# Optimization experiments

Hardware: AMD Instinct MI355X
Metric: run time of the kernel (lower is better)

The kernel has to match this reference:

```python
import jax, jax.numpy as jnp
import numpy as np

B, H, S, D = 4, 16, 4096, 64

def _phi(x):
    # feature map for linear attention: elu(x) + 1 (positive features)
    return jax.nn.elu(x) + 1.0

def setup_inputs() -> dict:
    key = jax.random.key(0)
    kq, kk, kv = jax.random.split(key, 3)
    return {
        "query": jax.random.normal(kq, (B, H, S, D), dtype=jnp.float32),
        "key": jax.random.normal(kk, (B, H, S, D), dtype=jnp.float32),
        "value": jax.random.normal(kv, (B, H, S, D), dtype=jnp.float32),
        "attention_mask": jnp.ones((B, S), dtype=jnp.float32),
    }

def reference(query, key, value, attention_mask):
    head_dim = query.shape[-1]
    scale = 1.0 / jnp.sqrt(jnp.sqrt(jnp.float32(head_dim)))
    q = query * scale
    k = key * scale
    phi_q = _phi(q)
    phi_k = _phi(k)
    m = attention_mask[:, None, :, None]  # [B,1,S,1]
    phi_q = phi_q * m
    phi_k = phi_k * m
    # kv_term: [B,H,D,Dv]
    kv_term = jnp.einsum("bhsd,bhse->bhde", phi_k, value)
    out = jnp.einsum("bhsd,bhde->bhse", phi_q, kv_term)
    # normalizer: phi_q @ sum_s phi_k -> [B,H,S,1]
    k_one = jnp.sum(phi_k, axis=-2)  # [B,H,D]
    normalizer = jnp.einsum("bhsd,bhd->bhs", phi_q, k_one)[..., None]
    return out / (normalizer + 1e-8)
```

## Files before the change

kernel.cpp:

```cpp
#include <hip/hip_runtime.h>

#define BDIM 4
#define HDIM 16
#define SDIM 4096
#define DDIM 64
#define NBH (BDIM * HDIM)

#define P1_TS 16
#define BH_STRIDE (DDIM * DDIM + DDIM)
#define CHUNK_FLOATS (NBH * BH_STRIDE)
#define P2_MT 128

__device__ __forceinline__ float phi_f(float x) {
    return x > 0.0f ? x + 1.0f : __expf(x);
}

template<bool ATOMIC>
__global__ __launch_bounds__(256) void la_phase1(
    const float* __restrict__ K, const float* __restrict__ V,
    const float* __restrict__ mask, float* __restrict__ outp, int chunk_rows)
{
    __shared__ float kT[2][P1_TS][DDIM];
    __shared__ float vT[2][P1_TS][DDIM];

    const int bh  = blockIdx.y;
    const int b   = bh / HDIM;
    const int t   = threadIdx.x;
    const int row = t >> 4;
    const int c4  = (t & 15) << 2;
    const int d0  = row << 2;
    const int e0  = c4;
    const int s_base = blockIdx.x * chunk_rows;

    const float* Kb = K + (size_t)bh * SDIM * DDIM;
    const float* Vb = V + (size_t)bh * SDIM * DDIM;
    const float* mb = mask + (size_t)b * SDIM;

    const float scale = 0.35355339059327373f;

    float acc[4][4] = {};
    float k1[4] = {0.f, 0.f, 0.f, 0.f};

    int s0 = s_base + row;
    float4 kf = *(const float4*)(Kb + (size_t)s0 * DDIM + c4);
    float4 vf = *(const float4*)(Vb + (size_t)s0 * DDIM + c4);
    float  m  = mb[s0];

    const int ntiles = chunk_rows >> 4;
    int p = 0;
    for (int tt = 0; tt < ntiles; ++tt) {
        const float p0 = phi_f(kf.x * scale) * m;
        const float p1 = phi_f(kf.y * scale) * m;
        const float p2 = phi_f(kf.z * scale) * m;
        const float p3 = phi_f(kf.w * scale) * m;
        kT[p][row][c4 + 0] = p0;
        kT[p][row][c4 + 1] = p1;
        kT[p][row][c4 + 2] = p2;
        kT[p][row][c4 + 3] = p3;
        *(float4*)&vT[p][row][c4] = vf;
        k1[0] += p0; k1[1] += p1; k1[2] += p2; k1[3] += p3;
        __syncthreads();

        if (tt + 1 < ntiles) {
            const int sn = s_base + ((tt + 1) << 4) + row;
            kf = *(const float4*)(Kb + (size_t)sn * DDIM + c4);
            vf = *(const float4*)(Vb + (size_t)sn * DDIM + c4);
            m  = mb[sn];
        }

        #pragma unroll
        for (int ss = 0; ss < P1_TS; ++ss) {
            const float4 a  = *(const float4*)&kT[p][ss][d0];
            const float4 v4 = *(const float4*)&vT[p][ss][e0];
            acc[0][0] += a.x * v4.x; acc[0][1] += a.x * v4.y; acc[0][2] += a.x * v4.z; acc[0][3] += a.x * v4.w;
            acc[1][0] += a.y * v4.x; acc[1][1] += a.y * v4.y; acc[1][2] += a.y * v4.z; acc[1][3] += a.y * v4.w;
            acc[2][0] += a.z * v4.x; acc[2][1] += a.z * v4.y; acc[2][2] += a.z * v4.z; acc[2][3] += a.z * v4.w;
            acc[3][0] += a.w * v4.x; acc[3][1] += a.w * v4.y; acc[3][2] += a.w * v4.z; acc[3][3] += a.w * v4.w;
        }
        p ^= 1;
    }

    float* base = ATOMIC ? (outp + (size_t)bh * BH_STRIDE)
                         : (outp + ((size_t)blockIdx.x * NBH + bh) * BH_STRIDE);
    if (ATOMIC) {
        #pragma unroll
        for (int i = 0; i < 4; ++i)
            #pragma unroll
            for (int j = 0; j < 4; ++j)
                atomicAdd(&base[(d0 + i) * DDIM + e0 + j], acc[i][j]);
    } else {
        #pragma unroll
        for (int i = 0; i < 4; ++i)
            *(float4*)&base[(d0 + i) * DDIM + e0] =
                make_float4(acc[i][0], acc[i][1], acc[i][2], acc[i][3]);
    }

    __syncthreads();
    kT[0][row][c4 + 0] = k1[0];
    kT[0][row][c4 + 1] = k1[1];
    kT[0][row][c4 + 2] = k1[2];
    kT[0][row][c4 + 3] = k1[3];
    __syncthreads();
    if (t < DDIM) {
        float s1 = 0.f;
        #pragma unroll
        for (int r = 0; r < P1_TS; ++r) s1 += kT[0][r][t];
        if (ATOMIC) atomicAdd(&base[DDIM * DDIM + t], s1);
        else        base[DDIM * DDIM + t] = s1;
    }
}

__global__ __launch_bounds__(256) void la_reduce(
    const float* __restrict__ part, float* __restrict__ fin, int nc)
{
    const int g = blockIdx.x * 256 + threadIdx.x;
    const float4* p4 = (const float4*)part;
    float4 s = p4[g];
    for (int c = 1; c < nc; ++c) {
        const float4 v = p4[(size_t)c * (CHUNK_FLOATS / 4) + g];
        s.x += v.x; s.y += v.y; s.z += v.z; s.w += v.w;
    }
    ((float4*)fin)[g] = s;
}

__global__ __launch_bounds__(512) void la_phase2(
    const float* __restrict__ Q, const float* __restrict__ mask,
    const float* __restrict__ fin_all, float* __restrict__ out)
{
    __shared__ float kvL[DDIM][DDIM];
    __shared__ float pqT[DDIM][P2_MT + 4];
    __shared__ float koL[DDIM];

    const int bh = blockIdx.y;
    const int b  = bh / HDIM;
    const int t  = threadIdx.x;
    const int s_base = blockIdx.x * P2_MT;

    const float scale = 0.35355339059327373f;
    const float* fin = fin_all + (size_t)bh * BH_STRIDE;

    {
        const float4* src = (const float4*)fin;
        float4* dst = (float4*)&kvL[0][0];
        dst[t] = src[t];
        dst[t + 512] = src[t + 512];
        if (t < DDIM) koL[t] = fin[DDIM * DDIM + t];
    }
    {
        const float* Qb = Q + (size_t)bh * SDIM * DDIM;
        const float* mb = mask + (size_t)b * SDIM;
        const int lr   = t & 15;
        const int c4   = ((t >> 4) & 15) << 2;
        const int half = t >> 8;
        #pragma unroll
        for (int k = 0; k < 4; ++k) {
            const int r = lr + 16 * (half * 4 + k);
            const int s = s_base + r;
            const float4 qf = *(const float4*)(Qb + (size_t)s * DDIM + c4);
            const float mm = mb[s];
            pqT[c4 + 0][r] = phi_f(qf.x * scale) * mm;
            pqT[c4 + 1][r] = phi_f(qf.y * scale) * mm;
            pqT[c4 + 2][r] = phi_f(qf.z * scale) * mm;
            pqT[c4 + 3][r] = phi_f(qf.w * scale) * mm;
        }
    }
    __syncthreads();

    const int r0 = (t >> 4) << 2;
    const int e0 = (t & 15) << 2;
    float acc[4][4] = {};
    float nrm[4] = {0.f, 0.f, 0.f, 0.f};

    #pragma unroll 16
    for (int d = 0; d < DDIM; ++d) {
        const float4 a  = *(const float4*)&pqT[d][r0];
        const float4 bb = *(const float4*)&kvL[d][e0];
        const float ko = koL[d];
        acc[0][0] += a.x * bb.x; acc[0][1] += a.x * bb.y; acc[0][2] += a.x * bb.z; acc[0][3] += a.x * bb.w;
        acc[1][0] += a.y * bb.x; acc[1][1] += a.y * bb.y; acc[1][2] += a.y * bb.z; acc[1][3] += a.y * bb.w;
        acc[2][0] += a.z * bb.x; acc[2][1] += a.z * bb.y; acc[2][2] += a.z * bb.z; acc[2][3] += a.z * bb.w;
        acc[3][0] += a.w * bb.x; acc[3][1] += a.w * bb.y; acc[3][2] += a.w * bb.z; acc[3][3] += a.w * bb.w;
        nrm[0] += a.x * ko; nrm[1] += a.y * ko; nrm[2] += a.z * ko; nrm[3] += a.w * ko;
    }

    float* ob = out + ((size_t)bh * SDIM + s_base) * DDIM;
    #pragma unroll
    for (int i = 0; i < 4; ++i) {
        const float inv = 1.0f / (nrm[i] + 1e-8f);
        float4 o;
        o.x = acc[i][0] * inv;
        o.y = acc[i][1] * inv;
        o.z = acc[i][2] * inv;
        o.w = acc[i][3] * inv;
        *(float4*)(ob + (size_t)(r0 + i) * DDIM + e0) = o;
    }
}

extern "C" void kernel_launch(void* const* d_in, const int* in_sizes, int n_in,
                              void* d_out, int out_size, void* d_ws, size_t ws_size,
                              hipStream_t stream) {
    const float* Q = (const float*)d_in[0];
    const float* K = (const float*)d_in[1];
    const float* V = (const float*)d_in[2];
    const float* M = (const float*)d_in[3];
    float* out = (float*)d_out;

    const size_t chunk_bytes = (size_t)CHUNK_FLOATS * sizeof(float);

    int nc = 0;
    if      (ws_size >= 33 * chunk_bytes) nc = 32;
    else if (ws_size >= 17 * chunk_bytes) nc = 16;

    if (nc > 0) {
        float* part = (float*)d_ws;
        float* fin  = part + (size_t)nc * CHUNK_FLOATS;
        la_phase1<false><<<dim3(nc, NBH), dim3(256), 0, stream>>>(K, V, M, part, SDIM / nc);
        la_reduce<<<dim3(CHUNK_FLOATS / 4 / 256), dim3(256), 0, stream>>>(part, fin, nc);
        la_phase2<<<dim3(SDIM / P2_MT, NBH), dim3(512), 0, stream>>>(Q, M, fin, out);
    } else {
        float* fin = (float*)d_ws;
        hipMemsetAsync(d_ws, 0, chunk_bytes, stream);
        la_phase1<true><<<dim3(16, NBH), dim3(256), 0, stream>>>(K, V, M, fin, SDIM / 16);
        la_phase2<<<dim3(SDIM / P2_MT, NBH), dim3(512), 0, stream>>>(Q, M, fin, out);
    }
}
```

Before: 248.0 us.

## Use 8x8 register tiles and per-wave independent pipelines in both phases

Phase 1 drops to 128 threads, two waves that each own half the chunk. Each wave has its own padded shared-memory tile, so the per-tile block barrier is gone, and each thread accumulates an 8x8 outer product. The two waves combine their results through shared memory at the end. Phase 2 likewise moves to 128 threads with 8x8 per-thread tiles, raising arithmetic intensity per shared-memory load at the cost of more registers and fewer threads per block, which may hurt latency hiding.

```diff
diff --git a/kernel.cpp b/kernel.cpp
--- a/kernel.cpp
+++ b/kernel.cpp
@@ -6,31 +6,41 @@
 #define DDIM 64
 #define NBH (BDIM * HDIM)
 
-#define P1_TS 16
 #define BH_STRIDE (DDIM * DDIM + DDIM)
 #define CHUNK_FLOATS (NBH * BH_STRIDE)
-#define P2_MT 128
+
+#define P1_STRIDE 66
+#define P1_WSZ (2 * 16 * P1_STRIDE)
 
 __device__ __forceinline__ float phi_f(float x) {
     return x > 0.0f ? x + 1.0f : __expf(x);
 }
 
 template<bool ATOMIC>
-__global__ __launch_bounds__(256) void la_phase1(
+__global__ __launch_bounds__(128) void la_phase1(
     const float* __restrict__ K, const float* __restrict__ V,
     const float* __restrict__ mask, float* __restrict__ outp, int chunk_rows)
 {
-    __shared__ float kT[2][P1_TS][DDIM];
-    __shared__ float vT[2][P1_TS][DDIM];
-
-    const int bh  = blockIdx.y;
-    const int b   = bh / HDIM;
-    const int t   = threadIdx.x;
-    const int row = t >> 4;
-    const int c4  = (t & 15) << 2;
-    const int d0  = row << 2;
-    const int e0  = c4;
-    const int s_base = blockIdx.x * chunk_rows;
+    __shared__ float smem[2 * P1_WSZ + 64];
+
+    const int bh = blockIdx.y;
+    const int b  = bh / HDIM;
+    const int t  = threadIdx.x;
+    const int w  = t >> 6;
+    const int l  = t & 63;
+
+    float* kTw = smem + w * P1_WSZ;
+    float* vTw = kTw + 16 * P1_STRIDE;
+    float* k1w = smem + 2 * P1_WSZ;
+
+    const int lr = l & 15;
+    const int cg = (l >> 4) << 2;
+    const int d0 = (l >> 3) << 3;
+    const int e0 = (l & 7) << 3;
+
+    const int rows_per_wave = chunk_rows >> 1;
+    const int s_wave = blockIdx.x * chunk_rows + w * rows_per_wave;
+    const int ntiles = rows_per_wave >> 4;
 
     const float* Kb = K + (size_t)bh * SDIM * DDIM;
     const float* Vb = V + (size_t)bh * SDIM * DDIM;
@@ -38,75 +48,113 @@
 
     const float scale = 0.35355339059327373f;
 
-    float acc[4][4] = {};
-    float k1[4] = {0.f, 0.f, 0.f, 0.f};
-
-    int s0 = s_base + row;
-    float4 kf = *(const float4*)(Kb + (size_t)s0 * DDIM + c4);
-    float4 vf = *(const float4*)(Vb + (size_t)s0 * DDIM + c4);
-    float  m  = mb[s0];
-
-    const int ntiles = chunk_rows >> 4;
-    int p = 0;
+    float acc[8][8] = {};
+    float k1p[4][4] = {};
+
+    float4 kf[4], vf[4];
+    float m;
+    {
+        const int sr = s_wave + lr;
+        #pragma unroll
+        for (int j = 0; j < 4; ++j) {
+            kf[j] = *(const float4*)(Kb + (size_t)sr * DDIM + cg + 16 * j);
+            vf[j] = *(const float4*)(Vb + (size_t)sr * DDIM + cg + 16 * j);
+        }
+        m = mb[sr];
+    }
+
     for (int tt = 0; tt < ntiles; ++tt) {
-        const float p0 = phi_f(kf.x * scale) * m;
-        const float p1 = phi_f(kf.y * scale) * m;
-        const float p2 = phi_f(kf.z * scale) * m;
-        const float p3 = phi_f(kf.w * scale) * m;
-        kT[p][row][c4 + 0] = p0;
-        kT[p][row][c4 + 1] = p1;
-        kT[p][row][c4 + 2] = p2;
-        kT[p][row][c4 + 3] = p3;
-        *(float4*)&vT[p][row][c4] = vf;
-        k1[0] += p0; k1[1] += p1; k1[2] += p2; k1[3] += p3;
-        __syncthreads();
-
+        float p[4][4];
+        #pragma unroll
+        for (int j = 0; j < 4; ++j) {
+            p[j][0] = phi_f(kf[j].x * scale) * m;
+            p[j][1] = phi_f(kf[j].y * scale) * m;
+            p[j][2] = phi_f(kf[j].z * scale) * m;
+            p[j][3] = phi_f(kf[j].w * scale) * m;
+            k1p[j][0] += p[j][0]; k1p[j][1] += p[j][1];
+            k1p[j][2] += p[j][2]; k1p[j][3] += p[j][3];
+        }
+        {
+            float* kw = kTw + lr * P1_STRIDE;
+            float* vw = vTw + lr * P1_STRIDE;
+            #pragma unroll
+            for (int j = 0; j < 4; ++j) {
+                const int c = cg + 16 * j;
+                *(float2*)(kw + c)     = make_float2(p[j][0], p[j][1]);
+                *(float2*)(kw + c + 2) = make_float2(p[j][2], p[j][3]);
+                *(float2*)(vw + c)     = make_float2(vf[j].x, vf[j].y);
+                *(float2*)(vw + c + 2) = make_float2(vf[j].z, vf[j].w);
+            }
+        }
         if (tt + 1 < ntiles) {
-            const int sn = s_base + ((tt + 1) << 4) + row;
-            kf = *(const float4*)(Kb + (size_t)sn * DDIM + c4);
-            vf = *(const float4*)(Vb + (size_t)sn * DDIM + c4);
-            m  = mb[sn];
-        }
-
-        #pragma unroll
-        for (int ss = 0; ss < P1_TS; ++ss) {
-            const float4 a  = *(const float4*)&kT[p][ss][d0];
-            const float4 v4 = *(const float4*)&vT[p][ss][e0];
-            acc[0][0] += a.x * v4.x; acc[0][1] += a.x * v4.y; acc[0][2] += a.x * v4.z; acc[0][3] += a.x * v4.w;
-            acc[1][0] += a.y * v4.x; acc[1][1] += a.y * v4.y; acc[1][2] += a.y * v4.z; acc[1][3] += a.y * v4.w;
-            acc[2][0] += a.z * v4.x; acc[2][1] += a.z * v4.y; acc[2][2] += a.z * v4.z; acc[2][3] += a.z * v4.w;
-            acc[3][0] += a.w * v4.x; acc[3][1] += a.w * v4.y; acc[3][2] += a.w * v4.z; acc[3][3] += a.w * v4.w;
-        }
-        p ^= 1;
-    }
-
-    float* base = ATOMIC ? (outp + (size_t)bh * BH_STRIDE)
-                         : (outp + ((size_t)blockIdx.x * NBH + bh) * BH_STRIDE);
-    if (ATOMIC) {
-        #pragma unroll
-        for (int i = 0; i < 4; ++i)
-            #pragma unroll
-            for (int j = 0; j < 4; ++j)
-                atomicAdd(&base[(d0 + i) * DDIM + e0 + j], acc[i][j]);
-    } else {
-        #pragma unroll
-        for (int i = 0; i < 4; ++i)
-            *(float4*)&base[(d0 + i) * DDIM + e0] =
-                make_float4(acc[i][0], acc[i][1], acc[i][2], acc[i][3]);
-    }
+            const int sr = s_wave + ((tt + 1) << 4) + lr;
+            #pragma unroll
+            for (int j = 0; j < 4; ++j) {
+                kf[j] = *(const float4*)(Kb + (size_t)sr * DDIM + cg + 16 * j);
+                vf[j] = *(const float4*)(Vb + (size_t)sr * DDIM + cg + 16 * j);
+            }
+            m = mb[sr];
+        }
+        #pragma unroll
+        for (int ss = 0; ss < 16; ++ss) {
+            float a[8], v[8];
+            const float* kr = kTw + ss * P1_STRIDE + d0;
+            const float* vr = vTw + ss * P1_STRIDE + e0;
+            *(float2*)&a[0] = *(const float2*)(kr);
+            *(float2*)&a[2] = *(const float2*)(kr + 2);
+            *(float2*)&a[4] = *(const float2*)(kr + 4);
+            *(float2*)&a[6] = *(const float2*)(kr + 6);
+            *(float2*)&v[0] = *(const float2*)(vr);
+            *(float2*)&v[2] = *(const float2*)(vr + 2);
+            *(float2*)&v[4] = *(const float2*)(vr + 4);
+            *(float2*)&v[6] = *(const float2*)(vr + 6);
+            #pragma unroll
+            for (int i = 0; i < 8; ++i)
+                #pragma unroll
+                for (int j = 0; j < 8; ++j)
+                    acc[i][j] += a[i] * v[j];
+        }
+    }
+
+    #pragma unroll
+    for (int j = 0; j < 4; ++j)
+        #pragma unroll
+        for (int jj = 0; jj < 4; ++jj)
+            kTw[lr * P1_STRIDE + cg + 16 * j + jj] = k1p[j][jj];
+    float k1s = 0.f;
+    #pragma unroll
+    for (int r = 0; r < 16; ++r) k1s += kTw[r * P1_STRIDE + l];
 
     __syncthreads();
-    kT[0][row][c4 + 0] = k1[0];
-    kT[0][row][c4 + 1] = k1[1];
-    kT[0][row][c4 + 2] = k1[2];
-    kT[0][row][c4 + 3] = k1[3];
+    float4* flat = (float4*)smem;
+    if (w == 1) {
+        #pragma unroll
+        for (int i = 0; i < 16; ++i) {
+            const int r = i >> 1, h = (i & 1) << 2;
+            flat[i * 64 + l] = make_float4(acc[r][h], acc[r][h + 1], acc[r][h + 2], acc[r][h + 3]);
+        }
+        k1w[l] = k1s;
+    }
     __syncthreads();
-    if (t < DDIM) {
-        float s1 = 0.f;
-        #pragma unroll
-        for (int r = 0; r < P1_TS; ++r) s1 += kT[0][r][t];
-        if (ATOMIC) atomicAdd(&base[DDIM * DDIM + t], s1);
-        else        base[DDIM * DDIM + t] = s1;
+    if (w == 0) {
+        float* base = ATOMIC ? (outp + (size_t)bh * BH_STRIDE)
+                             : (outp + ((size_t)blockIdx.x * NBH + bh) * BH_STRIDE);
+        #pragma unroll
+        for (int i = 0; i < 16; ++i) {
+            const int r = i >> 1, h = (i & 1) << 2;
+            float4 o = flat[i * 64 + l];
+            o.x += acc[r][h]; o.y += acc[r][h + 1]; o.z += acc[r][h + 2]; o.w += acc[r][h + 3];
+            if (ATOMIC) {
+                float* p = base + (d0 + r) * DDIM + e0 + h;
+                atomicAdd(p + 0, o.x); atomicAdd(p + 1, o.y);
+                atomicAdd(p + 2, o.z); atomicAdd(p + 3, o.w);
+            } else {
+                *(float4*)(base + (d0 + r) * DDIM + e0 + h) = o;
+            }
+        }
+        const float k1tot = k1s + k1w[l];
+        if (ATOMIC) atomicAdd(&base[DDIM * DDIM + l], k1tot);
+        else        base[DDIM * DDIM + l] = k1tot;
     }
 }
 
@@ -123,76 +171,75 @@
     ((float4*)fin)[g] = s;
 }
 
-__global__ __launch_bounds__(512) void la_phase2(
+__global__ __launch_bounds__(128) void la_phase2(
     const float* __restrict__ Q, const float* __restrict__ mask,
     const float* __restrict__ fin_all, float* __restrict__ out)
 {
-    __shared__ float kvL[DDIM][DDIM];
-    __shared__ float pqT[DDIM][P2_MT + 4];
+    __shared__ float kvL[DDIM * DDIM];
+    __shared__ float pqT[DDIM * 132];
     __shared__ float koL[DDIM];
 
     const int bh = blockIdx.y;
     const int b  = bh / HDIM;
     const int t  = threadIdx.x;
-    const int s_base = blockIdx.x * P2_MT;
+    const int s_base = blockIdx.x * 128;
 
     const float scale = 0.35355339059327373f;
     const float* fin = fin_all + (size_t)bh * BH_STRIDE;
 
     {
         const float4* src = (const float4*)fin;
-        float4* dst = (float4*)&kvL[0][0];
-        dst[t] = src[t];
-        dst[t + 512] = src[t + 512];
+        float4* dst = (float4*)kvL;
+        #pragma unroll
+        for (int i = 0; i < 8; ++i) dst[t + 128 * i] = src[t + 128 * i];
         if (t < DDIM) koL[t] = fin[DDIM * DDIM + t];
     }
     {
         const float* Qb = Q + (size_t)bh * SDIM * DDIM;
         const float* mb = mask + (size_t)b * SDIM;
-        const int lr   = t & 15;
-        const int c4   = ((t >> 4) & 15) << 2;
-        const int half = t >> 8;
-        #pragma unroll
-        for (int k = 0; k < 4; ++k) {
-            const int r = lr + 16 * (half * 4 + k);
-            const int s = s_base + r;
-            const float4 qf = *(const float4*)(Qb + (size_t)s * DDIM + c4);
-            const float mm = mb[s];
-            pqT[c4 + 0][r] = phi_f(qf.x * scale) * mm;
-            pqT[c4 + 1][r] = phi_f(qf.y * scale) * mm;
-            pqT[c4 + 2][r] = phi_f(qf.z * scale) * mm;
-            pqT[c4 + 3][r] = phi_f(qf.w * scale) * mm;
+        #pragma unroll
+        for (int j = 0; j < 16; ++j) {
+            const int row = (t & 15) + ((j & 7) << 4);
+            const int c4  = ((t >> 4) << 2) + ((j >> 3) << 5);
+            const float4 qf = *(const float4*)(Qb + (size_t)(s_base + row) * DDIM + c4);
+            const float mm = mb[s_base + row];
+            pqT[(c4 + 0) * 132 + row] = phi_f(qf.x * scale) * mm;
+            pqT[(c4 + 1) * 132 + row] = phi_f(qf.y * scale) * mm;
+            pqT[(c4 + 2) * 132 + row] = phi_f(qf.z * scale) * mm;
+            pqT[(c4 + 3) * 132 + row] = phi_f(qf.w * scale) * mm;
         }
     }
     __syncthreads();
 
-    const int r0 = (t >> 4) << 2;
-    const int e0 = (t & 15) << 2;
-    float acc[4][4] = {};
-    float nrm[4] = {0.f, 0.f, 0.f, 0.f};
-
-    #pragma unroll 16
+    const int r0 = (t >> 3) << 3;
+    const int e0 = (t & 7) << 3;
+    float acc[8][8] = {};
+    float nrm[8] = {};
+
+    #pragma unroll 4
     for (int d = 0; d < DDIM; ++d) {
-        const float4 a  = *(const float4*)&pqT[d][r0];
-        const float4 bb = *(const float4*)&kvL[d][e0];
+        float a[8], bb[8];
+        *(float4*)&a[0]  = *(const float4*)(pqT + d * 132 + r0);
+        *(float4*)&a[4]  = *(const float4*)(pqT + d * 132 + r0 + 4);
+        *(float4*)&bb[0] = *(const float4*)(kvL + d * DDIM + e0);
+        *(float4*)&bb[4] = *(const float4*)(kvL + d * DDIM + e0 + 4);
         const float ko = koL[d];
-        acc[0][0] += a.x * bb.x; acc[0][1] += a.x * bb.y; acc[0][2] += a.x * bb.z; acc[0][3] += a.x * bb.w;
-        acc[1][0] += a.y * bb.x; acc[1][1] += a.y * bb.y; acc[1][2] += a.y * bb.z; acc[1][3] += a.y * bb.w;
-        acc[2][0] += a.z * bb.x; acc[2][1] += a.z * bb.y; acc[2][2] += a.z * bb.z; acc[2][3] += a.z * bb.w;
-        acc[3][0] += a.w * bb.x; acc[3][1] += a.w * bb.y; acc[3][2] += a.w * bb.z; acc[3][3] += a.w * bb.w;
-        nrm[0] += a.x * ko; nrm[1] += a.y * ko; nrm[2] += a.z * ko; nrm[3] += a.w * ko;
+        #pragma unroll
+        for (int i = 0; i < 8; ++i) {
+            nrm[i] += a[i] * ko;
+            #pragma unroll
+            for (int j = 0; j < 8; ++j) acc[i][j] += a[i] * bb[j];
+        }
     }
 
     float* ob = out + ((size_t)bh * SDIM + s_base) * DDIM;
     #pragma unroll
-    for (int i = 0; i < 4; ++i) {
+    for (int i = 0; i < 8; ++i) {
         const float inv = 1.0f / (nrm[i] + 1e-8f);
-        float4 o;
-        o.x = acc[i][0] * inv;
-        o.y = acc[i][1] * inv;
-        o.z = acc[i][2] * inv;
-        o.w = acc[i][3] * inv;
-        *(float4*)(ob + (size_t)(r0 + i) * DDIM + e0) = o;
+        *(float4*)(ob + (size_t)(r0 + i) * DDIM + e0) =
+            make_float4(acc[i][0] * inv, acc[i][1] * inv, acc[i][2] * inv, acc[i][3] * inv);
+        *(float4*)(ob + (size_t)(r0 + i) * DDIM + e0 + 4) =
+            make_float4(acc[i][4] * inv, acc[i][5] * inv, acc[i][6] * inv, acc[i][7] * inv);
     }
 }
 
@@ -214,13 +261,13 @@
     if (nc > 0) {
         float* part = (float*)d_ws;
         float* fin  = part + (size_t)nc * CHUNK_FLOATS;
-        la_phase1<false><<<dim3(nc, NBH), dim3(256), 0, stream>>>(K, V, M, part, SDIM / nc);
+        la_phase1<false><<<dim3(nc, NBH), dim3(128), 0, stream>>>(K, V, M, part, SDIM / nc);
         la_reduce<<<dim3(CHUNK_FLOATS / 4 / 256), dim3(256), 0, stream>>>(part, fin, nc);
-        la_phase2<<<dim3(SDIM / P2_MT, NBH), dim3(512), 0, stream>>>(Q, M, fin, out);
+        la_phase2<<<dim3(SDIM / 128, NBH), dim3(128), 0, stream>>>(Q, M, fin, out);
     } else {
         float* fin = (float*)d_ws;
         hipMemsetAsync(d_ws, 0, chunk_bytes, stream);
-        la_phase1<true><<<dim3(16, NBH), dim3(256), 0, stream>>>(K, V, M, fin, SDIM / 16);
-        la_phase2<<<dim3(SDIM / P2_MT, NBH), dim3(512), 0, stream>>>(Q, M, fin, out);
-    }
-}
+        la_phase1<true><<<dim3(16, NBH), dim3(128), 0, stream>>>(K, V, M, fin, SDIM / 16);
+        la_phase2<<<dim3(SDIM / 128, NBH), dim3(128), 0, stream>>>(Q, M, fin, out);
+    }
+}
```

Result: slower. 266.3 us (+7.4%).
